# Optimization experiments

Hardware: AMD Instinct MI355X
Metric: run time of the kernel (lower is better)

Reference implementation:

```python
import jax, jax.numpy as jnp
import numpy as np

N_SCALES = 11
N_TAPS = 4
D4 = [0.4829629131445341, 0.8365163037378079, 0.2241438680420134, -0.1294095225512604]
B, N, D, H = 4, 2048, 1024, 16
HD = D // H  # 64


def setup_inputs() -> dict:
    key = jax.random.key(0)
    ks = jax.random.split(key, 8)
    s = 0.02
    return {
        "x": jax.random.normal(ks[0], (B, N, D), jnp.float32),
        "W_qkv": jax.random.normal(ks[1], (3 * D, D), jnp.float32) * s,
        "b_qkv": jnp.zeros((3 * D,), jnp.float32),
        "W_out": jax.random.normal(ks[2], (D, D), jnp.float32) * s,
        "b_out": jnp.zeros((D,), jnp.float32),
        "W_gate": jax.random.normal(ks[3], (D, D), jnp.float32) * s,
        "b_gate": jnp.full((D,), 2.0, jnp.float32),  # nn.init.constant_(gate bias, 2.0)
        "scale_gain": jax.random.normal(ks[4], (N_SCALES, H), jnp.float32) * 0.1,
        "W_qscale": jax.random.normal(ks[5], (N_SCALES, HD), jnp.float32) * 0.01,
        "identity_bypass": jnp.full((H,), -4.0, jnp.float32),
        "pos_bias": jax.random.normal(ks[6], (N_SCALES * N_TAPS, H), jnp.float32) * 0.01,
    }


def reference(x, W_qkv, b_qkv, W_out, b_out, W_gate, b_gate, scale_gain, W_qscale, identity_bypass, pos_bias):
    # qkv projection and head split -> [B,H,N,HD]
    qkv = x @ W_qkv.T + b_qkv
    q, k, v = jnp.split(qkv, 3, axis=-1)
    to_heads = lambda t: t.reshape(B, N, H, HD).transpose(0, 2, 1, 3)
    q, k, v = to_heads(q), to_heads(k), to_heads(v)

    # Q-conditioned per-scale gains: [B,H,N,n_scales]
    q_offset = jnp.einsum('bhnd,sd->bhns', q, W_qscale)
    prior = scale_gain.T[None, :, None, :]  # [1,H,1,S]
    gains = jax.nn.softmax(q_offset + prior, axis=-1)

    out = jnp.zeros((B, H, N, HD), q.dtype)
    z = jnp.zeros((B, H, N, 1), q.dtype)
    tap_idx = 0
    for j in range(N_SCALES):  # fixed small structural loop (44 taps total)
        d = 1 << j
        g_j = gains[..., j][..., None]  # [B,H,N,1]
        for tau, h_coef in enumerate(D4):
            offset = d * tau
            bias_jt = pos_bias[tap_idx].reshape(1, H, 1, 1)
            tap_idx += 1
            if offset != 0 and offset >= N:
                continue
            if offset == 0:
                k_s, v_s = k, v
            else:
                pad = jnp.zeros((B, H, offset, HD), k.dtype)
                k_s = jnp.concatenate([pad, k[:, :, :N - offset, :]], axis=2)
                v_s = jnp.concatenate([pad, v[:, :, :N - offset, :]], axis=2)
            qk_feat = jax.nn.elu(jnp.sum(q * k_s, -1, keepdims=True) + bias_jt) + 1.0
            out = out + (g_j * h_coef) * qk_feat * v_s
            z = z + g_j * abs(h_coef) * qk_feat

    # identity bypass (offset-0 local term)
    bypass = jax.nn.softplus(identity_bypass).reshape(1, H, 1, 1)
    local_ft = jax.nn.elu(jnp.sum(q * k, -1, keepdims=True)) + 1.0
    out = out + bypass * local_ft * v
    z = z + bypass * local_ft
    out = out / (z + 1e-06)

    gathered = out.transpose(0, 2, 1, 3).reshape(B, N, D)
    gate = jax.nn.sigmoid(x @ W_gate.T + b_gate)
    return (gathered * gate) @ W_out.T + b_out  # dropout p: eval mode -> identity
```

## Files before the change

### kernel.cpp

```cpp
#include <hip/hip_runtime.h>
#include <hip/hip_bf16.h>

#define PB 4
#define PN 2048
#define PD 1024
#define PH 16
#define PHD 64
#define NSC 11

typedef __attribute__((ext_vector_type(8))) short short8;
typedef __attribute__((ext_vector_type(4))) float floatx4;

#define AS1 __attribute__((address_space(1)))
#define AS3 __attribute__((address_space(3)))

static __device__ __forceinline__ unsigned short bf16bits(float f) {
    __hip_bfloat16 h = __float2bfloat16(f);
    return __builtin_bit_cast(unsigned short, h);
}

__global__ void cast_all(const float4* __restrict__ x,
                         const float4* __restrict__ wqkv,
                         const float4* __restrict__ wgate,
                         const float4* __restrict__ wout,
                         ushort4* __restrict__ x_bf,
                         ushort4* __restrict__ wcomb,
                         ushort4* __restrict__ woutb) {
    int i = blockIdx.x * blockDim.x + threadIdx.x;
    const int X4 = PB * PN * PD / 4;
    const int QKV4 = 3 * PD * PD / 4;
    const int G4 = PD * PD / 4;
    float4 v;
    ushort4* dst;
    if (i < X4) {
        v = x[i];
        dst = x_bf + i;
    } else {
        int j = i - X4;
        if (j < QKV4) {
            v = wqkv[j];
            dst = wcomb + j;
        } else if (j < QKV4 + G4) {
            v = wgate[j - QKV4];
            dst = wcomb + j;
        } else {
            v = wout[j - QKV4 - G4];
            dst = woutb + (j - QKV4 - G4);
        }
    }
    ushort4 o;
    o.x = bf16bits(v.x);
    o.y = bf16bits(v.y);
    o.z = bf16bits(v.z);
    o.w = bf16bits(v.w);
    *dst = o;
}

#define GBM 128
#define GBN 128
#define GBK 64

__global__ __launch_bounds__(256) void gemm_bt128(
    const __hip_bfloat16* __restrict__ A,
    const __hip_bfloat16* __restrict__ Bm,
    const float* __restrict__ b1,
    const float* __restrict__ b2,
    int split,
    float* __restrict__ out1, int N1,
    float* __restrict__ out2, int N2,
    int K) {
    __shared__ alignas(16) __hip_bfloat16 sA[GBM * GBK];
    __shared__ alignas(16) __hip_bfloat16 sB[GBN * GBK];

    const int tid = threadIdx.x;
    const int lane = tid & 63;
    const int wave = tid >> 6;
    const int wy = wave >> 1;
    const int wx = wave & 1;

    const int lrow8 = lane >> 3;
    const int lchunk = lane & 7;
    const int gchunk = lchunk ^ lrow8;

    const int r16 = lane & 15;
    const int qd = lane >> 4;
    const int sw = r16 & 7;

    floatx4 acc[4][4];
#pragma unroll
    for (int i = 0; i < 4; i++)
#pragma unroll
        for (int j = 0; j < 4; j++) acc[i][j] = (floatx4){0.f, 0.f, 0.f, 0.f};

    const size_t arow0 = (size_t)blockIdx.y * GBM;
    const size_t brow0 = (size_t)blockIdx.x * GBN;

    for (int k0 = 0; k0 < K; k0 += GBK) {
        __syncthreads();
#pragma unroll
        for (int half = 0; half < 4; half++) {
            const int rbase = wave * 8 + half * 32;
            const __hip_bfloat16* gA =
                A + (arow0 + rbase + lrow8) * K + k0 + gchunk * 8;
            __builtin_amdgcn_global_load_lds(
                (const AS1 unsigned int*)(const void*)gA,
                (AS3 unsigned int*)(void*)(sA + rbase * GBK), 16, 0, 0);
            const __hip_bfloat16* gB =
                Bm + (brow0 + rbase + lrow8) * K + k0 + gchunk * 8;
            __builtin_amdgcn_global_load_lds(
                (const AS1 unsigned int*)(const void*)gB,
                (AS3 unsigned int*)(void*)(sB + rbase * GBK), 16, 0, 0);
        }
        __syncthreads();

#pragma unroll
        for (int kk = 0; kk < 2; kk++) {
            short8 af[4], bf[4];
            const int cs = (qd + 4 * kk);
#pragma unroll
            for (int i = 0; i < 4; i++)
                af[i] = *(const short8*)(sA + (wy * 64 + i * 16 + r16) * GBK +
                                         ((cs ^ sw) * 8));
#pragma unroll
            for (int j = 0; j < 4; j++)
                bf[j] = *(const short8*)(sB + (wx * 64 + j * 16 + r16) * GBK +
                                         ((cs ^ sw) * 8));
#pragma unroll
            for (int i = 0; i < 4; i++)
#pragma unroll
                for (int j = 0; j < 4; j++)
                    acc[i][j] = __builtin_amdgcn_mfma_f32_16x16x32_bf16(
                        af[i], bf[j], acc[i][j], 0, 0, 0);
        }
    }

#pragma unroll
    for (int i = 0; i < 4; i++) {
#pragma unroll
        for (int j = 0; j < 4; j++) {
            const int colb = (int)brow0 + wx * 64 + j * 16 + r16;
            const bool first = colb < split;
            const float bb = first ? b1[colb] : b2[colb - split];
            float* dst = first ? out1 : out2;
            const int nn = first ? N1 : N2;
            const int cc = first ? colb : colb - split;
#pragma unroll
            for (int e = 0; e < 4; e++) {
                const size_t row = arow0 + wy * 64 + i * 16 + qd * 4 + e;
                dst[row * (size_t)nn + cc] = acc[i][j][e] + bb;
            }
        }
    }
}

#define TBM 256
#define TBN 256
#define TBK 64

__global__ __launch_bounds__(512) void gemm_bt256(
    const __hip_bfloat16* __restrict__ A,
    const __hip_bfloat16* __restrict__ Bm,
    const float* __restrict__ b1,
    const float* __restrict__ b2,
    int split,
    float* __restrict__ out1, int N1,
    float* __restrict__ out2, int N2,
    int K) {
    __shared__ alignas(16) __hip_bfloat16 sA[2 * TBM * TBK];
    __shared__ alignas(16) __hip_bfloat16 sB[2 * TBN * TBK];

    const int tid = threadIdx.x;
    const int lane = tid & 63;
    const int wid = tid >> 6;
    const int wrow = wid >> 2;
    const int wcol = wid & 3;

    const int lrow8 = lane >> 3;
    const int lchunk = lane & 7;
    const int gchunk = lchunk ^ lrow8;

    const int r16 = lane & 15;
    const int qd = lane >> 4;
    const int sw = r16 & 7;

    const int lin = blockIdx.x + (blockIdx.y << 4);
    const int swz = (lin & 7) * 64 + (lin >> 3);
    const int bx = swz & 15;
    const int by = swz >> 4;

    const size_t arow0 = (size_t)by * TBM;
    const size_t brow0 = (size_t)bx * TBN;

    const int nt = K >> 6;
    const size_t rowskip = (size_t)64 * K;

    const __hip_bfloat16* gA = A + (arow0 + wid * 8 + lrow8) * (size_t)K + gchunk * 8;
    const __hip_bfloat16* gB = Bm + (brow0 + wid * 8 + lrow8) * (size_t)K + gchunk * 8;
    const int ldsAb = wid * 8 * TBK;

    auto stage = [&](int cc, int ktn) {
#pragma unroll
        for (int rd = 0; rd < 4; ++rd) {
            __builtin_amdgcn_global_load_lds(
                (const AS1 unsigned int*)(const void*)(gA + (size_t)rd * rowskip + ktn * TBK),
                (AS3 unsigned int*)(void*)(sA + cc * (TBM * TBK) + ldsAb + rd * (64 * TBK)),
                16, 0, 0);
            __builtin_amdgcn_global_load_lds(
                (const AS1 unsigned int*)(const void*)(gB + (size_t)rd * rowskip + ktn * TBK),
                (AS3 unsigned int*)(void*)(sB + cc * (TBN * TBK) + ldsAb + rd * (64 * TBK)),
                16, 0, 0);
        }
    };

    floatx4 acc[8][4];
#pragma unroll
    for (int i = 0; i < 8; i++)
#pragma unroll
        for (int j = 0; j < 4; j++) acc[i][j] = (floatx4){0.f, 0.f, 0.f, 0.f};

    const int aofs = (wrow * 128 + r16) * TBK;
    const int bofs = (wcol * 64 + r16) * TBK;
    const int ck0 = ((qd ^ sw) * 8);
    const int ck1 = (((qd + 4) ^ sw) * 8);

    stage(0, 0);
    stage(1, 1);
    asm volatile("s_waitcnt vmcnt(8)" ::: "memory");
    __builtin_amdgcn_s_barrier();

#pragma unroll 1
    for (int kt = 0; kt < nt; ++kt) {
        const int c = kt & 1;
        const __hip_bfloat16* sAc = sA + c * (TBM * TBK);
        const __hip_bfloat16* sBc = sB + c * (TBN * TBK);

        short8 afr[8][2], bfr[4][2];

#pragma unroll
        for (int f = 0; f < 2; ++f) {
            bfr[f][0] = *(const short8*)(sBc + bofs + f * 1024 + ck0);
            bfr[f][1] = *(const short8*)(sBc + bofs + f * 1024 + ck1);
        }
#pragma unroll
        for (int f = 0; f < 4; ++f) {
            afr[f][0] = *(const short8*)(sAc + aofs + f * 1024 + ck0);
            afr[f][1] = *(const short8*)(sAc + aofs + f * 1024 + ck1);
        }
        __builtin_amdgcn_s_setprio(1);
#pragma unroll
        for (int i = 0; i < 4; ++i)
#pragma unroll
            for (int j = 0; j < 2; ++j)
#pragma unroll
                for (int kk = 0; kk < 2; ++kk)
                    acc[i][j] = __builtin_amdgcn_mfma_f32_16x16x32_bf16(
                        afr[i][kk], bfr[j][kk], acc[i][j], 0, 0, 0);
        __builtin_amdgcn_s_setprio(0);

#pragma unroll
        for (int f = 2; f < 4; ++f) {
            bfr[f][0] = *(const short8*)(sBc + bofs + f * 1024 + ck0);
            bfr[f][1] = *(const short8*)(sBc + bofs + f * 1024 + ck1);
        }
#pragma unroll
        for (int f = 4; f < 8; ++f) {
            afr[f][0] = *(const short8*)(sAc + aofs + f * 1024 + ck0);
            afr[f][1] = *(const short8*)(sAc + aofs + f * 1024 + ck1);
        }
        __builtin_amdgcn_s_setprio(1);
#pragma unroll
        for (int i = 0; i < 4; ++i)
#pragma unroll
            for (int j = 2; j < 4; ++j)
#pragma unroll
            for (int kk = 0; kk < 2; ++kk)
                    acc[i][j] = __builtin_amdgcn_mfma_f32_16x16x32_bf16(
                        afr[i][kk], bfr[j][kk], acc[i][j], 0, 0, 0);
        __builtin_amdgcn_s_setprio(0);

        asm volatile("s_waitcnt lgkmcnt(0)" ::: "memory");
        __builtin_amdgcn_sched_barrier(0);
        __builtin_amdgcn_s_barrier();

        if (kt + 2 < nt) stage(c, kt + 2);

        __builtin_amdgcn_s_setprio(1);
#pragma unroll
        for (int i = 4; i < 8; ++i)
#pragma unroll
            for (int j = 0; j < 2; ++j)
#pragma unroll
                for (int kk = 0; kk < 2; ++kk)
                    acc[i][j] = __builtin_amdgcn_mfma_f32_16x16x32_bf16(
                        afr[i][kk], bfr[j][kk], acc[i][j], 0, 0, 0);
        __builtin_amdgcn_s_setprio(0);

        __builtin_amdgcn_s_setprio(1);
#pragma unroll
        for (int i = 4; i < 8; ++i)
#pragma unroll
            for (int j = 2; j < 4; ++j)
#pragma unroll
                for (int kk = 0; kk < 2; ++kk)
                    acc[i][j] = __builtin_amdgcn_mfma_f32_16x16x32_bf16(
                        afr[i][kk], bfr[j][kk], acc[i][j], 0, 0, 0);
        __builtin_amdgcn_s_setprio(0);

        if (kt + 2 < nt) {
            asm volatile("s_waitcnt vmcnt(8)" ::: "memory");
        } else if (kt + 1 < nt) {
            asm volatile("s_waitcnt vmcnt(0)" ::: "memory");
        }
        if (kt + 1 < nt) __builtin_amdgcn_s_barrier();
    }

#pragma unroll
    for (int i = 0; i < 8; i++) {
#pragma unroll
        for (int j = 0; j < 4; j++) {
            const int colb = (int)brow0 + wcol * 64 + j * 16 + r16;
            const bool first = colb < split;
            const float bb = first ? b1[colb] : b2[colb - split];
            float* dst = first ? out1 : out2;
            const int nn = first ? N1 : N2;
            const int cc = first ? colb : colb - split;
#pragma unroll
            for (int e = 0; e < 4; e++) {
                const size_t row = arow0 + wrow * 128 + i * 16 + qd * 4 + e;
                dst[row * (size_t)nn + cc] = acc[i][j][e] + bb;
            }
        }
    }
}


static constexpr int OFFS[21] = {1, 2, 3, 4, 6, 8, 12, 16, 24, 32, 48,
                                 64, 96, 128, 192, 256, 384, 512, 768, 1024, 1536};
static constexpr int U1J[21] = {0, 0, 0, 1, 1, 2, 2, 3, 3, 4, 4,
                                5, 5, 6, 6, 7, 7, 8, 8, 9, 9};
static constexpr int U1T[21] = {1, 2, 3, 2, 3, 2, 3, 2, 3, 2, 3,
                                2, 3, 2, 3, 2, 3, 2, 3, 2, 3};
static constexpr int U2J[21] = {-1, 1, -1, 2, -1, 3, -1, 4, -1, 5, -1,
                                6, -1, 7, -1, 8, -1, 9, -1, 10, -1};

static __device__ __forceinline__ float red8(float s) {
    int t;
    t = __builtin_amdgcn_update_dpp(0, __builtin_bit_cast(int, s), 0xB1, 0xF, 0xF, true);
    s += __builtin_bit_cast(float, t);
    t = __builtin_amdgcn_update_dpp(0, __builtin_bit_cast(int, s), 0x4E, 0xF, 0xF, true);
    s += __builtin_bit_cast(float, t);
    t = __builtin_amdgcn_update_dpp(0, __builtin_bit_cast(int, s), 0x141, 0xF, 0xF, true);
    s += __builtin_bit_cast(float, t);
    return s;
}

__global__ __launch_bounds__(256) void attn_kernel(
    const float* __restrict__ qkv,
    const float* __restrict__ scale_gain,
    const float* __restrict__ W_qscale,
    const float* __restrict__ identity_bypass,
    const float* __restrict__ pos_bias,
    const float* __restrict__ gate,
    __hip_bfloat16* __restrict__ gated) {
    const int lane = threadIdx.x & 63;
    const int p = lane >> 3;
    const int l = lane & 7;

    const int wg = blockIdx.x;
    const int swg = (wg & 7) * 512 + (wg >> 3);

    const int flat = (swg * 4 + (threadIdx.x >> 6)) * 8;
    const int nbase = flat & (PN - 1);
    const int n = nbase + p;
    const int h = (flat >> 11) & (PH - 1);
    const int b = flat >> 15;

    const size_t base_bn = (size_t)b * PN;
    const int col = h * PHD + l * 8;

    const float* qp = qkv + (base_bn + n) * (3 * PD) + col;
    const float4 qa = *(const float4*)qp;
    const float4 qb = *(const float4*)(qp + 4);
    const float4 k0a = *(const float4*)(qp + PD);
    const float4 k0b = *(const float4*)(qp + PD + 4);
    const float4 v0a = *(const float4*)(qp + 2 * PD);
    const float4 v0b = *(const float4*)(qp + 2 * PD + 4);

    auto dot8 = [](float4 a0, float4 a1, float4 b0, float4 b1) {
        float s = a0.x * b0.x;
        s = fmaf(a0.y, b0.y, s);
        s = fmaf(a0.z, b0.z, s);
        s = fmaf(a0.w, b0.w, s);
        s = fmaf(a1.x, b1.x, s);
        s = fmaf(a1.y, b1.y, s);
        s = fmaf(a1.z, b1.z, s);
        s = fmaf(a1.w, b1.w, s);
        return red8(s);
    };

    const float dot0 = dot8(qa, qb, k0a, k0b);

    float g[NSC];
    float mx = -1e30f;
#pragma unroll
    for (int s = 0; s < NSC; s++) {
        const float* wp = W_qscale + s * PHD + l * 8;
        const float4 w0 = *(const float4*)wp;
        const float4 w1 = *(const float4*)(wp + 4);
        g[s] = dot8(qa, qb, w0, w1) + scale_gain[s * PH + h];
        mx = fmaxf(mx, g[s]);
    }
    float ssum = 0.f;
#pragma unroll
    for (int s = 0; s < NSC; s++) {
        g[s] = __expf(g[s] - mx);
        ssum += g[s];
    }
    const float inv = 1.f / ssum;
#pragma unroll
    for (int s = 0; s < NSC; s++) g[s] *= inv;

    const float D4c[4] = {0.4829629131445341f, 0.8365163037378079f,
                          0.2241438680420134f, -0.1294095225512604f};

    float4 o0, o1;
    float z;

    {
        const float bp = log1pf(__expf(identity_bypass[h]));
        const float f0 = (dot0 > 0.f ? dot0 : __expf(dot0) - 1.f) + 1.f;
        float wsum = bp * f0;
#pragma unroll
        for (int j = 0; j < NSC; j++) {
            const float xx = dot0 + pos_bias[(j * 4) * PH + h];
            const float feat = (xx > 0.f ? xx : __expf(xx) - 1.f) + 1.f;
            wsum = fmaf(g[j], D4c[0] * feat, wsum);
        }
        z = wsum;
        o0.x = wsum * v0a.x;
        o0.y = wsum * v0a.y;
        o0.z = wsum * v0a.z;
        o0.w = wsum * v0a.w;
        o1.x = wsum * v0b.x;
        o1.y = wsum * v0b.y;
        o1.z = wsum * v0b.z;
        o1.w = wsum * v0b.w;
    }

#pragma unroll
    for (int t = 0; t < 21; t++) {
        const int off = OFFS[t];
        if (off > nbase + 7) {
            {
                const int j = U1J[t], tau = U1T[t];
                const float xx = pos_bias[(j * 4 + tau) * PH + h];
                const float feat = (xx > 0.f ? xx : __expf(xx) - 1.f) + 1.f;
                z = fmaf(g[j] * fabsf(D4c[tau]), feat, z);
            }
            if (U2J[t] >= 0) {
                const int j = U2J[t];
                const float xx = pos_bias[(j * 4 + 1) * PH + h];
                const float feat = (xx > 0.f ? xx : __expf(xx) - 1.f) + 1.f;
                z = fmaf(g[j] * D4c[1], feat, z);
            }
        } else {
            const bool valid = (n >= off);
            const int idx = valid ? (n - off) : 0;
            const float vm = valid ? 1.f : 0.f;
            const size_t rb = (base_bn + idx) * (3 * PD);
            const float* kp = qkv + rb + PD + col;
            const float* vp = qkv + rb + 2 * PD + col;
            const float4 k4a = *(const float4*)kp;
            const float4 k4b = *(const float4*)(kp + 4);
            const float4 v4a = *(const float4*)vp;
            const float4 v4b = *(const float4*)(vp + 4);
            const float dv = dot8(qa, qb, k4a, k4b) * vm;

            float wv, zacc;
            {
                const int j = U1J[t], tau = U1T[t];
                const float xx = dv + pos_bias[(j * 4 + tau) * PH + h];
                const float feat = (xx > 0.f ? xx : __expf(xx) - 1.f) + 1.f;
                const float wp = g[j] * (D4c[tau] * feat);
                zacc = fabsf(wp);
                wv = wp;
            }
            if (U2J[t] >= 0) {
                const int j = U2J[t];
                const float xx = dv + pos_bias[(j * 4 + 1) * PH + h];
                const float feat = (xx > 0.f ? xx : __expf(xx) - 1.f) + 1.f;
                const float wp = g[j] * (D4c[1] * feat);
                zacc += wp;
                wv += wp;
            }
            z += zacc;
            wv *= vm;
            o0.x = fmaf(wv, v4a.x, o0.x);
            o0.y = fmaf(wv, v4a.y, o0.y);
            o0.z = fmaf(wv, v4a.z, o0.z);
            o0.w = fmaf(wv, v4a.w, o0.w);
            o1.x = fmaf(wv, v4b.x, o1.x);
            o1.y = fmaf(wv, v4b.y, o1.y);
            o1.z = fmaf(wv, v4b.z, o1.z);
            o1.w = fmaf(wv, v4b.w, o1.w);
        }
    }

    const float* gp2 = gate + (base_bn + n) * PD + col;
    const float4 ga = *(const float4*)gp2;
    const float4 gb = *(const float4*)(gp2 + 4);
    const float zi = 1.f / (z + 1e-6f);

    short8 r;
    r[0] = (short)bf16bits(o0.x * zi / (1.f + __expf(-ga.x)));
    r[1] = (short)bf16bits(o0.y * zi / (1.f + __expf(-ga.y)));
    r[2] = (short)bf16bits(o0.z * zi / (1.f + __expf(-ga.z)));
    r[3] = (short)bf16bits(o0.w * zi / (1.f + __expf(-ga.w)));
    r[4] = (short)bf16bits(o1.x * zi / (1.f + __expf(-gb.x)));
    r[5] = (short)bf16bits(o1.y * zi / (1.f + __expf(-gb.y)));
    r[6] = (short)bf16bits(o1.z * zi / (1.f + __expf(-gb.z)));
    r[7] = (short)bf16bits(o1.w * zi / (1.f + __expf(-gb.w)));
    *(short8*)(gated + (base_bn + n) * PD + col) = r;
}

extern "C" void kernel_launch(void* const* d_in, const int* in_sizes, int n_in,
                              void* d_out, int out_size, void* d_ws, size_t ws_size,
                              hipStream_t stream) {
    const float* x = (const float*)d_in[0];
    const float* W_qkv = (const float*)d_in[1];
    const float* b_qkv = (const float*)d_in[2];
    const float* W_out = (const float*)d_in[3];
    const float* b_out = (const float*)d_in[4];
    const float* W_gate = (const float*)d_in[5];
    const float* b_gate = (const float*)d_in[6];
    const float* scale_gain = (const float*)d_in[7];
    const float* W_qscale = (const float*)d_in[8];
    const float* identity_bypass = (const float*)d_in[9];
    const float* pos_bias = (const float*)d_in[10];
    float* out = (float*)d_out;

    const int M = PB * PN;
    char* ws = (char*)d_ws;
    size_t off = 0;
    auto alloc = [&](size_t bytes) -> void* {
        void* p = ws + off;
        off += (bytes + 255) & ~(size_t)255;
        return p;
    };
    __hip_bfloat16* x_bf = (__hip_bfloat16*)alloc((size_t)M * PD * 2);
    __hip_bfloat16* wcomb_bf = (__hip_bfloat16*)alloc((size_t)4 * PD * PD * 2);
    __hip_bfloat16* wout_bf = (__hip_bfloat16*)alloc((size_t)PD * PD * 2);
    float* qkv = (float*)alloc((size_t)M * 3 * PD * 4);
    float* gate = (float*)alloc((size_t)M * PD * 4);
    __hip_bfloat16* gated = (__hip_bfloat16*)alloc((size_t)M * PD * 2);

    const int TOT4 = M * PD / 4 + 5 * PD * PD / 4;
    cast_all<<<TOT4 / 256, 256, 0, stream>>>(
        (const float4*)x, (const float4*)W_qkv, (const float4*)W_gate,
        (const float4*)W_out, (ushort4*)x_bf, (ushort4*)wcomb_bf,
        (ushort4*)wout_bf);

    gemm_bt256<<<dim3(4 * PD / TBN, M / TBM), 512, 0, stream>>>(
        x_bf, wcomb_bf, b_qkv, b_gate, 3 * PD, qkv, 3 * PD, gate, PD, PD);

    attn_kernel<<<(PB * PH * PN) / 32, 256, 0, stream>>>(
        qkv, scale_gain, W_qscale, identity_bypass, pos_bias, gate, gated);

    gemm_bt128<<<dim3(PD / GBN, M / GBM), 256, 0, stream>>>(
        gated, wout_bf, b_out, b_out, PD, out, PD, out, PD, PD);
}
```

Before: 292.4 us.

## Replace output-projection GEMM with double-buffered 256x128 pipelined kernel

The final output projection GEMM switches from a single-buffered 128x128 tile kernel with 256 threads to a 256x128 tile kernel with 512 threads. The new kernel double-buffers LDS, prefetches two K-tiles ahead, interleaves MFMA groups with the global-to-LDS loads, and raises wave priority around the MFMA groups. It also remaps block indices to improve L2 reuse. The aim is to hide global load latency and cut barrier stalls. The grid shrinks from 512 to 256 blocks, which may leave compute units underused on a large GPU.

```diff
diff --git a/kernel.cpp b/kernel.cpp
--- a/kernel.cpp
+++ b/kernel.cpp
@@ -56,103 +56,6 @@
     *dst = o;
 }
 
-#define GBM 128
-#define GBN 128
-#define GBK 64
-
-__global__ __launch_bounds__(256) void gemm_bt128(
-    const __hip_bfloat16* __restrict__ A,
-    const __hip_bfloat16* __restrict__ Bm,
-    const float* __restrict__ b1,
-    const float* __restrict__ b2,
-    int split,
-    float* __restrict__ out1, int N1,
-    float* __restrict__ out2, int N2,
-    int K) {
-    __shared__ alignas(16) __hip_bfloat16 sA[GBM * GBK];
-    __shared__ alignas(16) __hip_bfloat16 sB[GBN * GBK];
-
-    const int tid = threadIdx.x;
-    const int lane = tid & 63;
-    const int wave = tid >> 6;
-    const int wy = wave >> 1;
-    const int wx = wave & 1;
-
-    const int lrow8 = lane >> 3;
-    const int lchunk = lane & 7;
-    const int gchunk = lchunk ^ lrow8;
-
-    const int r16 = lane & 15;
-    const int qd = lane >> 4;
-    const int sw = r16 & 7;
-
-    floatx4 acc[4][4];
-#pragma unroll
-    for (int i = 0; i < 4; i++)
-#pragma unroll
-        for (int j = 0; j < 4; j++) acc[i][j] = (floatx4){0.f, 0.f, 0.f, 0.f};
-
-    const size_t arow0 = (size_t)blockIdx.y * GBM;
-    const size_t brow0 = (size_t)blockIdx.x * GBN;
-
-    for (int k0 = 0; k0 < K; k0 += GBK) {
-        __syncthreads();
-#pragma unroll
-        for (int half = 0; half < 4; half++) {
-            const int rbase = wave * 8 + half * 32;
-            const __hip_bfloat16* gA =
-                A + (arow0 + rbase + lrow8) * K + k0 + gchunk * 8;
-            __builtin_amdgcn_global_load_lds(
-                (const AS1 unsigned int*)(const void*)gA,
-                (AS3 unsigned int*)(void*)(sA + rbase * GBK), 16, 0, 0);
-            const __hip_bfloat16* gB =
-                Bm + (brow0 + rbase + lrow8) * K + k0 + gchunk * 8;
-            __builtin_amdgcn_global_load_lds(
-                (const AS1 unsigned int*)(const void*)gB,
-                (AS3 unsigned int*)(void*)(sB + rbase * GBK), 16, 0, 0);
-        }
-        __syncthreads();
-
-#pragma unroll
-        for (int kk = 0; kk < 2; kk++) {
-            short8 af[4], bf[4];
-            const int cs = (qd + 4 * kk);
-#pragma unroll
-            for (int i = 0; i < 4; i++)
-                af[i] = *(const short8*)(sA + (wy * 64 + i * 16 + r16) * GBK +
-                                         ((cs ^ sw) * 8));
-#pragma unroll
-            for (int j = 0; j < 4; j++)
-                bf[j] = *(const short8*)(sB + (wx * 64 + j * 16 + r16) * GBK +
-                                         ((cs ^ sw) * 8));
-#pragma unroll
-            for (int i = 0; i < 4; i++)
-#pragma unroll
-                for (int j = 0; j < 4; j++)
-                    acc[i][j] = __builtin_amdgcn_mfma_f32_16x16x32_bf16(
-                        af[i], bf[j], acc[i][j], 0, 0, 0);
-        }
-    }
-
-#pragma unroll
-    for (int i = 0; i < 4; i++) {
-#pragma unroll
-        for (int j = 0; j < 4; j++) {
-            const int colb = (int)brow0 + wx * 64 + j * 16 + r16;
-            const bool first = colb < split;
-            const float bb = first ? b1[colb] : b2[colb - split];
-            float* dst = first ? out1 : out2;
-            const int nn = first ? N1 : N2;
-            const int cc = first ? colb : colb - split;
-#pragma unroll
-            for (int e = 0; e < 4; e++) {
-                const size_t row = arow0 + wy * 64 + i * 16 + qd * 4 + e;
-                dst[row * (size_t)nn + cc] = acc[i][j][e] + bb;
-            }
-        }
-    }
-}
-
 #define TBM 256
 #define TBN 256
 #define TBK 64
@@ -328,6 +231,173 @@
             for (int e = 0; e < 4; e++) {
                 const size_t row = arow0 + wrow * 128 + i * 16 + qd * 4 + e;
                 dst[row * (size_t)nn + cc] = acc[i][j][e] + bb;
+            }
+        }
+    }
+}
+
+#define UBM 256
+#define UBN 128
+#define UBK 64
+
+__global__ __launch_bounds__(512) void gemm_bt256x128(
+    const __hip_bfloat16* __restrict__ A,
+    const __hip_bfloat16* __restrict__ Bm,
+    const float* __restrict__ bias,
+    float* __restrict__ out, int N1, int K) {
+    __shared__ alignas(16) __hip_bfloat16 sA[2 * UBM * UBK];
+    __shared__ alignas(16) __hip_bfloat16 sB[2 * UBN * UBK];
+
+    const int tid = threadIdx.x;
+    const int lane = tid & 63;
+    const int wid = tid >> 6;
+    const int wrow = wid >> 2;
+    const int wcol = wid & 3;
+
+    const int lrow8 = lane >> 3;
+    const int gchunk = (lane & 7) ^ lrow8;
+
+    const int r16 = lane & 15;
+    const int qd = lane >> 4;
+    const int sw = r16 & 7;
+
+    const int lin = blockIdx.x + (blockIdx.y << 3);
+    const int swz = (lin & 7) * 32 + (lin >> 3);
+    const int bx = swz & 7;
+    const int by = swz >> 3;
+
+    const size_t arow0 = (size_t)by * UBM;
+    const size_t brow0 = (size_t)bx * UBN;
+
+    const int nt = K >> 6;
+    const size_t rowskip = (size_t)64 * K;
+
+    const __hip_bfloat16* gA = A + (arow0 + wid * 8 + lrow8) * (size_t)K + gchunk * 8;
+    const __hip_bfloat16* gB = Bm + (brow0 + wid * 8 + lrow8) * (size_t)K + gchunk * 8;
+    const int ldsAb = wid * 8 * UBK;
+
+    auto stage = [&](int cc, int ktn) {
+#pragma unroll
+        for (int rd = 0; rd < 4; ++rd)
+            __builtin_amdgcn_global_load_lds(
+                (const AS1 unsigned int*)(const void*)(gA + (size_t)rd * rowskip + ktn * UBK),
+                (AS3 unsigned int*)(void*)(sA + cc * (UBM * UBK) + ldsAb + rd * (64 * UBK)),
+                16, 0, 0);
+#pragma unroll
+        for (int rd = 0; rd < 2; ++rd)
+            __builtin_amdgcn_global_load_lds(
+                (const AS1 unsigned int*)(const void*)(gB + (size_t)rd * rowskip + ktn * UBK),
+                (AS3 unsigned int*)(void*)(sB + cc * (UBN * UBK) + ldsAb + rd * (64 * UBK)),
+                16, 0, 0);
+    };
+
+    floatx4 acc[8][2];
+#pragma unroll
+    for (int i = 0; i < 8; i++)
+#pragma unroll
+        for (int j = 0; j < 2; j++) acc[i][j] = (floatx4){0.f, 0.f, 0.f, 0.f};
+
+    const int aofs = (wrow * 128 + r16) * UBK;
+    const int bofs = (wcol * 32 + r16) * UBK;
+    const int ck0 = ((qd ^ sw) * 8);
+    const int ck1 = (((qd + 4) ^ sw) * 8);
+
+    stage(0, 0);
+    stage(1, 1);
+    asm volatile("s_waitcnt vmcnt(6)" ::: "memory");
+    __builtin_amdgcn_s_barrier();
+
+#pragma unroll 1
+    for (int kt = 0; kt < nt; ++kt) {
+        const int c = kt & 1;
+        const __hip_bfloat16* sAc = sA + c * (UBM * UBK);
+        const __hip_bfloat16* sBc = sB + c * (UBN * UBK);
+
+        short8 afr[8][2], bfr[2][2];
+
+#pragma unroll
+        for (int f = 0; f < 2; ++f) {
+            bfr[f][0] = *(const short8*)(sBc + bofs + f * 1024 + ck0);
+            bfr[f][1] = *(const short8*)(sBc + bofs + f * 1024 + ck1);
+        }
+#pragma unroll
+        for (int f = 0; f < 4; ++f) {
+            afr[f][0] = *(const short8*)(sAc + aofs + f * 1024 + ck0);
+            afr[f][1] = *(const short8*)(sAc + aofs + f * 1024 + ck1);
+        }
+        __builtin_amdgcn_s_setprio(1);
+#pragma unroll
+        for (int i = 0; i < 2; ++i)
+#pragma unroll
+            for (int j = 0; j < 2; ++j)
+#pragma unroll
+                for (int kk = 0; kk < 2; ++kk)
+                    acc[i][j] = __builtin_amdgcn_mfma_f32_16x16x32_bf16(
+                        afr[i][kk], bfr[j][kk], acc[i][j], 0, 0, 0);
+        __builtin_amdgcn_s_setprio(0);
+
+#pragma unroll
+        for (int f = 4; f < 8; ++f) {
+            afr[f][0] = *(const short8*)(sAc + aofs + f * 1024 + ck0);
+            afr[f][1] = *(const short8*)(sAc + aofs + f * 1024 + ck1);
+        }
+        __builtin_amdgcn_s_setprio(1);
+#pragma unroll
+        for (int i = 2; i < 4; ++i)
+#pragma unroll
+            for (int j = 0; j < 2; ++j)
+#pragma unroll
+                for (int kk = 0; kk < 2; ++kk)
+                    acc[i][j] = __builtin_amdgcn_mfma_f32_16x16x32_bf16(
+                        afr[i][kk], bfr[j][kk], acc[i][j], 0, 0, 0);
+        __builtin_amdgcn_s_setprio(0);
+
+        asm volatile("s_waitcnt lgkmcnt(0)" ::: "memory");
+        __builtin_amdgcn_sched_barrier(0);
+        __builtin_amdgcn_s_barrier();
+
+        if (kt + 2 < nt) stage(c, kt + 2);
+
+        __builtin_amdgcn_s_setprio(1);
+#pragma unroll
+        for (int i = 4; i < 6; ++i)
+#pragma unroll
+            for (int j = 0; j < 2; ++j)
+#pragma unroll
+                for (int kk = 0; kk < 2; ++kk)
+                    acc[i][j] = __builtin_amdgcn_mfma_f32_16x16x32_bf16(
+                        afr[i][kk], bfr[j][kk], acc[i][j], 0, 0, 0);
+        __builtin_amdgcn_s_setprio(0);
+
+        __builtin_amdgcn_s_setprio(1);
+#pragma unroll
+        for (int i = 6; i < 8; ++i)
+#pragma unroll
+            for (int j = 0; j < 2; ++j)
+#pragma unroll
+                for (int kk = 0; kk < 2; ++kk)
+                    acc[i][j] = __builtin_amdgcn_mfma_f32_16x16x32_bf16(
+                        afr[i][kk], bfr[j][kk], acc[i][j], 0, 0, 0);
+        __builtin_amdgcn_s_setprio(0);
+
+        if (kt + 2 < nt) {
+            asm volatile("s_waitcnt vmcnt(6)" ::: "memory");
+        } else if (kt + 1 < nt) {
+            asm volatile("s_waitcnt vmcnt(0)" ::: "memory");
+        }
+        if (kt + 1 < nt) __builtin_amdgcn_s_barrier();
+    }
+
+#pragma unroll
+    for (int i = 0; i < 8; i++) {
+#pragma unroll
+        for (int j = 0; j < 2; j++) {
+            const int colb = (int)brow0 + wcol * 32 + j * 16 + r16;
+            const float bb = bias[colb];
+#pragma unroll
+            for (int e = 0; e < 4; e++) {
+                const size_t row = arow0 + wrow * 128 + i * 16 + qd * 4 + e;
+                out[row * (size_t)N1 + colb] = acc[i][j][e] + bb;
             }
         }
     }
@@ -566,6 +636,6 @@
     attn_kernel<<<(PB * PH * PN) / 32, 256, 0, stream>>>(
         qkv, scale_gain, W_qscale, identity_bypass, pos_bias, gate, gated);
 
-    gemm_bt128<<<dim3(PD / GBN, M / GBM), 256, 0, stream>>>(
-        gated, wout_bf, b_out, b_out, PD, out, PD, out, PD, PD);
+    gemm_bt256x128<<<dim3(PD / UBN, M / UBM), 512, 0, stream>>>(
+        gated, wout_bf, b_out, out, PD, PD);
 }
```

Result: faster. 286.0 us (-2.2%).
